# Kernel optimization log

Measured on AMD Instinct MI355X. Metric: run time of the kernel, lower is better.

The kernel has to match this reference:

```python
import jax, jax.numpy as jnp
import numpy as np

C = 512
G = 32  # groups
EPS = 1e-6

def setup_inputs() -> dict:
    key = jax.random.key(0)
    ks = jax.random.split(key, 12)
    x = jax.random.normal(ks[0], (2, C, 64, 64), dtype=jnp.float32)
    s = 1.0 / np.sqrt(C)
    params = {
        'gn_scale': jnp.ones((C,), jnp.float32),
        'gn_bias': jnp.zeros((C,), jnp.float32),
        'wq': jax.random.normal(ks[1], (C, C), jnp.float32) * s,
        'bq': jax.random.normal(ks[2], (C,), jnp.float32) * 0.01,
        'wk': jax.random.normal(ks[3], (C, C), jnp.float32) * s,
        'bk': jax.random.normal(ks[4], (C,), jnp.float32) * 0.01,
        'wv': jax.random.normal(ks[5], (C, C), jnp.float32) * s,
        'bv': jax.random.normal(ks[6], (C,), jnp.float32) * 0.01,
        'wp': jax.random.normal(ks[7], (C, C), jnp.float32) * s,
        'bp': jax.random.normal(ks[8], (C,), jnp.float32) * 0.01,
    }
    return {'x': x, **params}


def _group_norm(x, scale, bias):
    b, c, h, w = x.shape
    xg = x.reshape(b, G, c // G, h, w)
    mean = jnp.mean(xg, axis=(2, 3, 4), keepdims=True)
    var = jnp.var(xg, axis=(2, 3, 4), keepdims=True)
    xg = (xg - mean) * jax.lax.rsqrt(var + EPS)
    x = xg.reshape(b, c, h, w)
    return x * scale[None, :, None, None] + bias[None, :, None, None]


def _conv1x1(x, w, bias):
    # x: [b,c,h,w], w: [out,in] -> [b,out,h,w]
    return jnp.einsum('oc,bchw->bohw', w, x) + bias[None, :, None, None]


def reference(x, gn_scale, gn_bias, wq, bq, wk, bk, wv, bv, wp, bp):
    h = _group_norm(x, gn_scale, gn_bias)
    q = _conv1x1(h, wq, bq)
    k = _conv1x1(h, wk, bk)
    v = _conv1x1(h, wv, bv)
    b, c, h_, w_ = q.shape
    n = h_ * w_
    q = q.reshape(b, c, n)
    k = k.reshape(b, c, n)
    v = v.reshape(b, c, n)
    # attn[b,i,j] = sum_c q[b,c,i] k[b,c,j] * c^-0.5
    attn = jnp.einsum('bci,bcj->bij', q, k) * (c ** -0.5)
    attn = jax.nn.softmax(attn, axis=2)
    # out[b,c,i] = sum_j v[b,c,j] attn[b,i,j]
    out = jnp.einsum('bcj,bij->bci', v, attn)
    out = out.reshape(b, c, h_, w_)
    out = _conv1x1(out, wp, bp)
    return x + out
```

## Files before the change

### kernel.cpp

```cpp
#include <hip/hip_runtime.h>
#include <stdint.h>

typedef short short8 __attribute__((ext_vector_type(8)));
typedef short short4v __attribute__((ext_vector_type(4)));
typedef float f32x4 __attribute__((ext_vector_type(4)));
typedef float float4v __attribute__((ext_vector_type(4)));

__device__ inline float bf2f(short s) {
    union { unsigned u; float f; } c;
    c.u = ((unsigned)(unsigned short)s) << 16;
    return c.f;
}
__device__ inline short f2bf(float f) {
    union { float f; unsigned u; } c;
    c.f = f;
    unsigned u = c.u;
    unsigned r = (u + 0x7fffu + ((u >> 16) & 1u)) >> 16;
    return (short)r;
}

typedef const __attribute__((address_space(1))) char GChar;
typedef __attribute__((address_space(3))) char LChar;
__device__ __forceinline__ void gload_lds16(const void* g, void* l) {
    __builtin_amdgcn_global_load_lds((GChar*)g, (LChar*)l, 16, 0, 0);
}

template<int N> __device__ __forceinline__ void wait_vm() {
    if constexpr (N == 0)      asm volatile("s_waitcnt vmcnt(0)" ::: "memory");
    else if constexpr (N == 4) asm volatile("s_waitcnt vmcnt(4)" ::: "memory");
    else if constexpr (N == 6) asm volatile("s_waitcnt vmcnt(6)" ::: "memory");
    else static_assert(N == 0 || N == 4 || N == 6, "unsupported vmcnt");
}

__device__ __forceinline__ void wait_lgkm0() {
    asm volatile("s_waitcnt lgkmcnt(0)" ::: "memory");
}
__device__ __forceinline__ void wait_lgkm8() {
    asm volatile("s_waitcnt lgkmcnt(8)" ::: "memory");
}

__device__ __forceinline__ void phase_barrier() {
    __builtin_amdgcn_s_barrier();
    asm volatile("" ::: "memory");
}

__device__ __forceinline__ void swz_xy(int& bx, int& by) {
    int gx = gridDim.x;
    int nwg = gx * gridDim.y;
    int wg = by * gx + bx;
    int chunk = nwg >> 3;
    int swz = (wg & 7) * chunk + (wg >> 3);
    bx = swz % gx;
    by = swz / gx;
}

__global__ __launch_bounds__(256) void conv_w4(const float* __restrict__ w0, const float* __restrict__ w1,
                                               const float* __restrict__ w2, const float* __restrict__ w3,
                                               short* __restrict__ dst, float s0,
                                               float* __restrict__ rowsum,
                                               const float* __restrict__ bq, const float* __restrict__ bk,
                                               float* __restrict__ bqk, float* __restrict__ statsraw) {
    int gid = blockIdx.x * 256 + threadIdx.x;
    if (gid < 8192) rowsum[gid] = 0.0f;
    if (gid < 128)  statsraw[gid] = 0.0f;
    if (gid < 1024) bqk[gid] = (gid < 512) ? bq[gid] * s0 : bk[gid - 512];
    int idx = gid * 4;
    int wi = idx >> 18;
    int off = idx & 262143;
    const float* src = (wi == 0) ? w0 : (wi == 1) ? w1 : (wi == 2) ? w2 : w3;
    float sc = (wi == 0) ? s0 : 1.0f;
    float4v v = *reinterpret_cast<const float4v*>(src + off);
    short4v o;
    o[0] = f2bf(v[0] * sc); o[1] = f2bf(v[1] * sc);
    o[2] = f2bf(v[2] * sc); o[3] = f2bf(v[3] * sc);
    *reinterpret_cast<short4v*>(dst + idx) = o;
}

__global__ __launch_bounds__(256) void gn_stats2(const float* __restrict__ x, float* __restrict__ statsraw) {
    int bg = blockIdx.x;
    const float* p = x + (size_t)bg * 65536 + blockIdx.y * 8192;
    float s = 0.f, ss = 0.f;
    #pragma unroll
    for (int i = threadIdx.x * 4; i < 8192; i += 1024) {
        float4v q = *reinterpret_cast<const float4v*>(p + i);
        s  += q[0] + q[1] + q[2] + q[3];
        ss += q[0]*q[0] + q[1]*q[1] + q[2]*q[2] + q[3]*q[3];
    }
    #pragma unroll
    for (int off = 32; off >= 1; off >>= 1) {
        s  += __shfl_xor(s, off);
        ss += __shfl_xor(ss, off);
    }
    __shared__ float rs[8];
    int w = threadIdx.x >> 6, lane = threadIdx.x & 63;
    if (lane == 0) { rs[w] = s; rs[4 + w] = ss; }
    __syncthreads();
    if (threadIdx.x == 0) {
        float S1 = rs[0] + rs[1] + rs[2] + rs[3];
        float S2 = rs[4] + rs[5] + rs[6] + rs[7];
        atomicAdd(&statsraw[bg * 2],     S1);
        atomicAdd(&statsraw[bg * 2 + 1], S2);
    }
}

__global__ __launch_bounds__(256) void gn_apply_t(const float* __restrict__ x, const float* __restrict__ statsraw,
                                                  const float* __restrict__ scale, const float* __restrict__ bias,
                                                  short* __restrict__ hT) {
    __shared__ float t[64][65];
    int n0 = blockIdx.x * 64, c0 = blockIdx.y * 64, b = blockIdx.z;
    const float* xb = x + (size_t)b * 512 * 4096;
    int col = threadIdx.x & 63, rb = threadIdx.x >> 6;
    #pragma unroll
    for (int r = 0; r < 16; ++r) {
        int cl = rb + r * 4;
        int c = c0 + cl;
        int g = c >> 4;
        float sum   = statsraw[(b * 32 + g) * 2];
        float sumsq = statsraw[(b * 32 + g) * 2 + 1];
        float mean = sum * (1.f / 65536.f);
        float var  = sumsq * (1.f / 65536.f) - mean * mean;
        float rstd = rsqrtf(var + 1e-6f);
        float v = xb[(size_t)c * 4096 + n0 + col];
        t[col][cl] = (v - mean) * rstd * scale[c] + bias[c];
    }
    __syncthreads();
    short* hb = hT + (size_t)b * 4096 * 512;
    #pragma unroll
    for (int r = 0; r < 16; ++r) {
        int nl = rb + r * 4;
        hb[(size_t)(n0 + nl) * 512 + c0 + col] = f2bf(t[nl][col]);
    }
}

template<int EPI>
__global__ __launch_bounds__(512, 2) void gemm8b(
    const short* __restrict__ A, int zdiv, long sAb1, long sAb2, int lda,
    const short* __restrict__ B, long sBb1, long sBb2, int ldb,
    short* __restrict__ C, long sCb1, long sCb2, int ldc,
    int K, float* __restrict__ rowsum)
{
    __shared__ __align__(16) char lds[131072];

    const int tid = threadIdx.x;
    int bx = blockIdx.x, by = blockIdx.y;
    swz_xy(bx, by);
    const int bm = bx * 256, bn = by * 256;
    const int zb = blockIdx.z / zdiv, zs = blockIdx.z % zdiv;

    const short* Ab = A + (size_t)zb * sAb1 + (size_t)zs * sAb2;
    const short* Bb = B + (size_t)zb * sBb1 + (size_t)zs * sBb2;

    const int w = tid >> 6, lane = tid & 63;
    const int wm = w >> 2, wn = w & 3;
    const int l15 = lane & 15, l4 = lane >> 4;

    long srcAh[2][2], srcBh[2][2]; int dstAh[2][2], dstBh[2][2];
    #pragma unroll
    for (int h = 0; h < 2; ++h) {
        #pragma unroll
        for (int i = 0; i < 2; ++i) {
            int ch = i * 512 + tid;
            int r = h * 128 + (ch >> 3), c = ch & 7;
            srcAh[h][i] = (long)(bm + r) * lda + ((c ^ (r & 7)) << 3);
            dstAh[h][i] = r * 128 + c * 16;
            srcBh[h][i] = (long)(bn + r) * ldb + ((c ^ (r & 7)) << 3);
            dstBh[h][i] = 32768 + r * 128 + c * 16;
        }
    }
    auto stageAh = [&](int buf, int h, long kt) {
        char* l = lds + buf * 65536;
        gload_lds16(Ab + srcAh[h][0] + kt, l + dstAh[h][0]);
        gload_lds16(Ab + srcAh[h][1] + kt, l + dstAh[h][1]);
    };
    auto stageBh = [&](int buf, int h, long kt) {
        char* l = lds + buf * 65536;
        gload_lds16(Bb + srcBh[h][0] + kt, l + dstBh[h][0]);
        gload_lds16(Bb + srcBh[h][1] + kt, l + dstBh[h][1]);
    };

    auto fragA = [&](const char* base, int m, int ks) -> short8 {
        int r = wm * 128 + m * 16 + l15;
        int kk = ks * 4 + l4;
        return *reinterpret_cast<const short8*>(base + r * 128 + ((kk * 16) ^ ((r & 7) << 4)));
    };
    auto fragB = [&](const char* base, int n, int ks) -> short8 {
        int r = wn * 64 + n * 16 + l15;
        int kk = ks * 4 + l4;
        return *reinterpret_cast<const short8*>(base + 32768 + r * 128 + ((kk * 16) ^ ((r & 7) << 4)));
    };

    f32x4 acc[8][4] = {};
    const int nk = K >> 6;

    stageBh(0, 0, 0); stageBh(0, 1, 0);
    stageAh(0, 0, 0); stageAh(0, 1, 0);
    if (nk > 1) {
        stageBh(1, 0, 64); stageBh(1, 1, 64);
        wait_vm<4>();
    } else {
        wait_vm<0>();
    }
    phase_barrier();

    short8 bf[4][2];

    for (int t = 0; t < nk; ++t) {
        const char* lr = lds + (t & 1) * 65536;
        const int bufN = (t & 1) ^ 1;
        const int bufT = (t & 1);
        const long ktA = (long)(t + 1) << 6;
        const long ktB = (long)(t + 2) << 6;
        const bool pA = (t + 1 < nk);
        const bool pB = (t + 2 < nk);
        short8 a00, a01, a10, a11;

        #pragma unroll
        for (int n = 0; n < 4; ++n) { bf[n][0] = fragB(lr, n, 0); bf[n][1] = fragB(lr, n, 1); }
        a00 = fragA(lr, 0, 0); a01 = fragA(lr, 0, 1);
        a10 = fragA(lr, 1, 0); a11 = fragA(lr, 1, 1);
        if (pA) stageAh(bufN, 0, ktA);
        wait_lgkm8();
        phase_barrier();
        wait_lgkm0();
        __builtin_amdgcn_s_setprio(1);
        #pragma unroll
        for (int n = 0; n < 4; ++n) {
            acc[0][n] = __builtin_amdgcn_mfma_f32_16x16x32_bf16(a00, bf[n][0], acc[0][n], 0, 0, 0);
            acc[0][n] = __builtin_amdgcn_mfma_f32_16x16x32_bf16(a01, bf[n][1], acc[0][n], 0, 0, 0);
            acc[1][n] = __builtin_amdgcn_mfma_f32_16x16x32_bf16(a10, bf[n][0], acc[1][n], 0, 0, 0);
            acc[1][n] = __builtin_amdgcn_mfma_f32_16x16x32_bf16(a11, bf[n][1], acc[1][n], 0, 0, 0);
        }
        __builtin_amdgcn_s_setprio(0);
        __builtin_amdgcn_sched_barrier(0);
        phase_barrier();

        a00 = fragA(lr, 2, 0); a01 = fragA(lr, 2, 1);
        a10 = fragA(lr, 3, 0); a11 = fragA(lr, 3, 1);
        if (pA) stageAh(bufN, 1, ktA);
        phase_barrier();
        wait_lgkm0();
        __builtin_amdgcn_s_setprio(1);
        #pragma unroll
        for (int n = 0; n < 4; ++n) {
            acc[2][n] = __builtin_amdgcn_mfma_f32_16x16x32_bf16(a00, bf[n][0], acc[2][n], 0, 0, 0);
            acc[2][n] = __builtin_amdgcn_mfma_f32_16x16x32_bf16(a01, bf[n][1], acc[2][n], 0, 0, 0);
            acc[3][n] = __builtin_amdgcn_mfma_f32_16x16x32_bf16(a10, bf[n][0], acc[3][n], 0, 0, 0);
            acc[3][n] = __builtin_amdgcn_mfma_f32_16x16x32_bf16(a11, bf[n][1], acc[3][n], 0, 0, 0);
        }
        __builtin_amdgcn_s_setprio(0);
        __builtin_amdgcn_sched_barrier(0);
        phase_barrier();

        a00 = fragA(lr, 4, 0); a01 = fragA(lr, 4, 1);
        a10 = fragA(lr, 5, 0); a11 = fragA(lr, 5, 1);
        if (pB) stageBh(bufT, 0, ktB);
        phase_barrier();
        wait_lgkm0();
        __builtin_amdgcn_s_setprio(1);
        #pragma unroll
        for (int n = 0; n < 4; ++n) {
            acc[4][n] = __builtin_amdgcn_mfma_f32_16x16x32_bf16(a00, bf[n][0], acc[4][n], 0, 0, 0);
            acc[4][n] = __builtin_amdgcn_mfma_f32_16x16x32_bf16(a01, bf[n][1], acc[4][n], 0, 0, 0);
            acc[5][n] = __builtin_amdgcn_mfma_f32_16x16x32_bf16(a10, bf[n][0], acc[5][n], 0, 0, 0);
            acc[5][n] = __builtin_amdgcn_mfma_f32_16x16x32_bf16(a11, bf[n][1], acc[5][n], 0, 0, 0);
        }
        __builtin_amdgcn_s_setprio(0);
        __builtin_amdgcn_sched_barrier(0);
        phase_barrier();

        a00 = fragA(lr, 6, 0); a01 = fragA(lr, 6, 1);
        a10 = fragA(lr, 7, 0); a11 = fragA(lr, 7, 1);
        if (pB) stageBh(bufT, 1, ktB);
        if (pB)      wait_vm<4>();
        else if (pA) wait_vm<0>();
        phase_barrier();
        wait_lgkm0();
        __builtin_amdgcn_s_setprio(1);
        #pragma unroll
        for (int n = 0; n < 4; ++n) {
            acc[6][n] = __builtin_amdgcn_mfma_f32_16x16x32_bf16(a00, bf[n][0], acc[6][n], 0, 0, 0);
            acc[6][n] = __builtin_amdgcn_mfma_f32_16x16x32_bf16(a01, bf[n][1], acc[6][n], 0, 0, 0);
            acc[7][n] = __builtin_amdgcn_mfma_f32_16x16x32_bf16(a10, bf[n][0], acc[7][n], 0, 0, 0);
            acc[7][n] = __builtin_amdgcn_mfma_f32_16x16x32_bf16(a11, bf[n][1], acc[7][n], 0, 0, 0);
        }
        __builtin_amdgcn_s_setprio(0);
        __builtin_amdgcn_sched_barrier(0);
        phase_barrier();
    }

    short* Cb = C + (size_t)zb * sCb1 + (size_t)zs * sCb2;
    if constexpr (EPI == 0) {
        #pragma unroll
        for (int m = 0; m < 8; ++m) {
            #pragma unroll
            for (int r = 0; r < 4; ++r) {
                int row = bm + wm * 128 + m * 16 + l4 * 4 + r;
                #pragma unroll
                for (int n = 0; n < 4; ++n) {
                    int col = bn + wn * 64 + n * 16 + l15;
                    Cb[(size_t)row * ldc + col] = f2bf(acc[m][n][r]);
                }
            }
        }
    } else if constexpr (EPI == 2) {
        #pragma unroll
        for (int m = 0; m < 8; ++m) {
            #pragma unroll
            for (int r = 0; r < 4; ++r) {
                int row = bm + wm * 128 + m * 16 + l4 * 4 + r;
                float inv = 1.0f / rowsum[zb * 4096 + row];
                #pragma unroll
                for (int n = 0; n < 4; ++n) {
                    int col = bn + wn * 64 + n * 16 + l15;
                    Cb[(size_t)row * ldc + col] = f2bf(acc[m][n][r] * inv);
                }
            }
        }
    } else {
        float* lsum = (float*)lds;
        #pragma unroll
        for (int m = 0; m < 8; ++m) {
            #pragma unroll
            for (int r = 0; r < 4; ++r) {
                int lrow = wm * 128 + m * 16 + l4 * 4 + r;
                int row = bm + lrow;
                float part = 0.0f;
                #pragma unroll
                for (int n = 0; n < 4; ++n) {
                    int col = bn + wn * 64 + n * 16 + l15;
                    float e = __expf(acc[m][n][r]);
                    part += e;
                    Cb[(size_t)row * ldc + col] = f2bf(e);
                }
                part += __shfl_xor(part, 1);
                part += __shfl_xor(part, 2);
                part += __shfl_xor(part, 4);
                part += __shfl_xor(part, 8);
                if (l15 == 0) lsum[wn * 256 + lrow] = part;
            }
        }
        __syncthreads();
        if (tid < 256) {
            float s = (lsum[tid] + lsum[256 + tid]) + (lsum[512 + tid] + lsum[768 + tid]);
            atomicAdd(&rowsum[zb * 4096 + bm + tid], s);
        }
    }
}

template<int BMT, int BNT, int WM, int WN>
__global__ __launch_bounds__(512) void gemm_nt3(
    const short* __restrict__ A, int zdiv, long sAb1, long sAb2, int lda,
    const short* __restrict__ B, long sBb1, long sBb2, int ldb,
    void* __restrict__ Cv, long sCb1, long sCb2, int ldc,
    int K,
    const float* __restrict__ bias, int bias_mode,
    const float* __restrict__ res, long sResb,
    int c_fp32)
{
    constexpr int BUFB = (BMT + BNT) * 128;
    constexpr int ALPT = BMT / 64;
    constexpr int BLPT = BNT / 64;
    constexpr int MF   = BMT / WM / 16;
    constexpr int NF   = BNT / WN / 16;
    __shared__ __align__(16) char lds[2 * BUFB];

    const int tid = threadIdx.x;
    int bx = blockIdx.x, by = blockIdx.y;
    swz_xy(bx, by);
    const int bm = bx * BMT;
    const int bn = by * BNT;
    const int bz = blockIdx.z;
    const int zb = bz / zdiv, zs = bz % zdiv;

    const short* Ab = A + (size_t)zb * sAb1 + (size_t)zs * sAb2;
    const short* Bb = B + (size_t)zb * sBb1 + (size_t)zs * sBb2;

    const int w = tid >> 6;
    const int lane = tid & 63;
    const int wm = w / WN, wn = w % WN;
    const int wr = wm * (BMT / WM);
    const int wc = wn * (BNT / WN);

    f32x4 acc[MF][NF] = {};
    const int nk = K >> 6;

    auto stage = [&](int buf, int kt) {
        char* la = lds + buf * BUFB;
        char* lb = la + BMT * 128;
        #pragma unroll
        for (int i = 0; i < ALPT; ++i) {
            int ch = i * 512 + tid;
            int r = ch >> 3, c = ch & 7;
            gload_lds16(Ab + (size_t)(bm + r) * lda + kt + ((c ^ (r & 7)) << 3), la + ch * 16);
        }
        #pragma unroll
        for (int i = 0; i < BLPT; ++i) {
            int ch = i * 512 + tid;
            int r = ch >> 3, c = ch & 7;
            gload_lds16(Bb + (size_t)(bn + r) * ldb + kt + ((c ^ (r & 7)) << 3), lb + ch * 16);
        }
    };

    stage(0, 0);
    int cur = 0;
    for (int t = 0; t < nk; ++t) {
        if (t + 1 < nk) {
            stage(cur ^ 1, (t + 1) << 6);
            wait_vm<6>();
        } else {
            wait_vm<0>();
        }
        phase_barrier();

        const char* la = lds + cur * BUFB;
        const char* lb = la + BMT * 128;
        #pragma unroll
        for (int ks = 0; ks < 2; ++ks) {
            const int kb = ks * 64 + (lane >> 4) * 16;
            short8 af[MF], bfv[NF];
            #pragma unroll
            for (int m = 0; m < MF; ++m) {
                int r = wr + m * 16 + (lane & 15);
                af[m] = *reinterpret_cast<const short8*>(la + r * 128 + (kb ^ ((r & 7) << 4)));
            }
            #pragma unroll
            for (int n = 0; n < NF; ++n) {
                int r = wc + n * 16 + (lane & 15);
                bfv[n] = *reinterpret_cast<const short8*>(lb + r * 128 + (kb ^ ((r & 7) << 4)));
            }
            #pragma unroll
            for (int m = 0; m < MF; ++m)
                #pragma unroll
                for (int n = 0; n < NF; ++n)
                    acc[m][n] = __builtin_amdgcn_mfma_f32_16x16x32_bf16(af[m], bfv[n], acc[m][n], 0, 0, 0);
        }
        asm volatile("" ::: "memory");
        __builtin_amdgcn_s_barrier();
        cur ^= 1;
    }

    const int row0 = (lane >> 4) * 4;
    const int col0 = lane & 15;
    short* Cb16 = (short*)Cv + (size_t)zb * sCb1 + (size_t)zs * sCb2;
    float* Cf32 = (float*)Cv + (size_t)zb * sCb1 + (size_t)zs * sCb2;
    const float* resb = res ? res + (size_t)zb * sResb : nullptr;

    #pragma unroll
    for (int m = 0; m < MF; ++m) {
        #pragma unroll
        for (int r = 0; r < 4; ++r) {
            int row = bm + wr + m * 16 + row0 + r;
            float bvr = (bias_mode == 1) ? bias[row] : 0.0f;
            #pragma unroll
            for (int n = 0; n < NF; ++n) {
                int col = bn + wc + n * 16 + col0;
                float v = acc[m][n][r];
                if (bias_mode == 1) v += bvr;
                else if (bias_mode == 2) v += bias[col];
                size_t idx = (size_t)row * ldc + col;
                if (c_fp32) {
                    if (resb) v += resb[idx];
                    Cf32[idx] = v;
                } else {
                    Cb16[idx] = f2bf(v);
                }
            }
        }
    }
}

template<int BNT>
__global__ __launch_bounds__(256) void gemm_nt2(
    const short* __restrict__ A, long sAb, int lda,
    const short* __restrict__ B, long sBb, int ldb,
    void* __restrict__ Cv, long sCb, int ldc,
    int K,
    const float* __restrict__ bias, int bias_mode,
    const float* __restrict__ res, long sResb,
    int c_fp32)
{
    constexpr int BMT = 128;
    constexpr int NF  = BNT / 32;
    constexpr int BUF = (BMT + BNT) * 128;
    constexpr int ALPT = (BMT * 8) / 256;
    constexpr int BLPT = (BNT * 8) / 256;
    __shared__ __align__(16) char lds[2 * BUF];

    const int tid = threadIdx.x;
    int bx = blockIdx.x, by = blockIdx.y;
    swz_xy(bx, by);
    const int bm = bx * BMT;
    const int bn = by * BNT;
    const int bz = blockIdx.z;

    const short* Ab = A + (size_t)bz * sAb;
    const short* Bb = B + (size_t)bz * sBb;

    const int w = tid >> 6;
    const int lane = tid & 63;
    const int wr = (w >> 1) * 64;
    const int wc = (w & 1) * (BNT / 2);

    f32x4 acc[4][NF] = {};
    const int nk = K >> 6;

    auto stage = [&](int buf, int kt) {
        char* la = lds + buf * BUF;
        char* lb = la + BMT * 128;
        #pragma unroll
        for (int i = 0; i < ALPT; ++i) {
            int ch = i * 256 + tid;
            int r = ch >> 3, c = ch & 7;
            gload_lds16(Ab + (size_t)(bm + r) * lda + kt + ((c ^ (r & 7)) << 3), la + ch * 16);
        }
        #pragma unroll
        for (int i = 0; i < BLPT; ++i) {
            int ch = i * 256 + tid;
            int r = ch >> 3, c = ch & 7;
            gload_lds16(Bb + (size_t)(bn + r) * ldb + kt + ((c ^ (r & 7)) << 3), lb + ch * 16);
        }
    };

    stage(0, 0);
    int cur = 0;
    for (int t = 0; t < nk; ++t) {
        if (t + 1 < nk) {
            stage(cur ^ 1, (t + 1) << 6);
            wait_vm<6>();
        } else {
            wait_vm<0>();
        }
        phase_barrier();

        const char* la = lds + cur * BUF;
        const char* lb = la + BMT * 128;
        #pragma unroll
        for (int ks = 0; ks < 2; ++ks) {
            const int kb = ks * 64 + (lane >> 4) * 16;
            short8 af[4], bfv[NF];
            #pragma unroll
            for (int m = 0; m < 4; ++m) {
                int r = wr + m * 16 + (lane & 15);
                af[m] = *reinterpret_cast<const short8*>(la + r * 128 + (kb ^ ((r & 7) << 4)));
            }
            #pragma unroll
            for (int n = 0; n < NF; ++n) {
                int r = wc + n * 16 + (lane & 15);
                bfv[n] = *reinterpret_cast<const short8*>(lb + r * 128 + (kb ^ ((r & 7) << 4)));
            }
            #pragma unroll
            for (int m = 0; m < 4; ++m)
                #pragma unroll
                for (int n = 0; n < NF; ++n)
                    acc[m][n] = __builtin_amdgcn_mfma_f32_16x16x32_bf16(af[m], bfv[n], acc[m][n], 0, 0, 0);
        }
        asm volatile("" ::: "memory");
        __builtin_amdgcn_s_barrier();
        cur ^= 1;
    }

    const int row0 = (lane >> 4) * 4;
    const int col0 = lane & 15;
    short* Cb16 = (short*)Cv + (size_t)bz * sCb;
    float* Cf32 = (float*)Cv + (size_t)bz * sCb;
    const float* resb = res ? res + (size_t)bz * sResb : nullptr;

    #pragma unroll
    for (int m = 0; m < 4; ++m) {
        #pragma unroll
        for (int r = 0; r < 4; ++r) {
            int row = bm + wr + m * 16 + row0 + r;
            float bvr = (bias_mode == 1) ? bias[row] : 0.0f;
            #pragma unroll
            for (int n = 0; n < NF; ++n) {
                int col = bn + wc + n * 16 + col0;
                float v = acc[m][n][r];
                if (bias_mode == 1) v += bvr;
                else if (bias_mode == 2) v += bias[col];
                size_t idx = (size_t)row * ldc + col;
                if (c_fp32) {
                    if (resb) v += resb[idx];
                    Cf32[idx] = v;
                } else {
                    Cb16[idx] = f2bf(v);
                }
            }
        }
    }
}

__global__ __launch_bounds__(256) void gemm_out(
    const short* __restrict__ A,
    const short* __restrict__ part, long sPz, long sPb,
    float* __restrict__ Cout, long sCb, int ldc,
    const float* __restrict__ bias,
    const float* __restrict__ res, long sResb)
{
    constexpr int BMT = 128, BNT = 64;
    constexpr int BUF = (BMT + BNT) * 128;
    __shared__ __align__(16) char lds[2 * BUF];

    const int tid = threadIdx.x;
    int bx = blockIdx.x, by = blockIdx.y;
    swz_xy(bx, by);
    const int bm = bx * BMT;
    const int bn = by * BNT;
    const int bz = blockIdx.z;

    const short* Pb = part + (size_t)bz * sPb;

    const int w = tid >> 6;
    const int lane = tid & 63;
    const int wr = (w >> 1) * 64;
    const int wc = (w & 1) * 32;

    f32x4 acc[4][2] = {};
    const int nk = 8;

    long srcA[4]; int dstA[4];
    #pragma unroll
    for (int i = 0; i < 4; ++i) {
        int ch = i * 256 + tid;
        int r = ch >> 3, c = ch & 7;
        srcA[i] = (long)(bm + r) * 512 + ((c ^ (r & 7)) << 3);
        dstA[i] = ch * 16;
    }
    long srcB[2]; int dstB[2];
    #pragma unroll
    for (int i = 0; i < 2; ++i) {
        int ch = i * 256 + tid;
        int r = ch >> 3, c = ch & 7;
        srcB[i] = (long)(bn + r) * 512 + c * 8;
        dstB[i] = BMT * 128 + r * 128 + ((c * 16) ^ ((r & 7) << 4));
    }

    auto stageA = [&](int buf, long kt) {
        char* la = lds + buf * BUF;
        #pragma unroll
        for (int i = 0; i < 4; ++i) gload_lds16(A + srcA[i] + kt, la + dstA[i]);
    };
    auto loadB = [&](long kt, short8 rv[2][4]) {
        #pragma unroll
        for (int i = 0; i < 2; ++i)
            #pragma unroll
            for (int z = 0; z < 4; ++z)
                rv[i][z] = *reinterpret_cast<const short8*>(Pb + z * sPz + srcB[i] + kt);
    };
    auto writeB = [&](int buf, short8 rv[2][4]) {
        char* l = lds + buf * BUF;
        #pragma unroll
        for (int i = 0; i < 2; ++i) {
            short8 o;
            #pragma unroll
            for (int j = 0; j < 8; ++j)
                o[j] = f2bf((bf2f(rv[i][0][j]) + bf2f(rv[i][1][j])) +
                            (bf2f(rv[i][2][j]) + bf2f(rv[i][3][j])));
            *reinterpret_cast<short8*>(l + dstB[i]) = o;
        }
    };

    short8 rv[2][4];
    stageA(0, 0);
    loadB(0, rv);
    writeB(0, rv);
    __syncthreads();

    int cur = 0;
    for (int t = 0; t < nk; ++t) {
        const bool pA = (t + 1 < nk);
        if (pA) {
            stageA(cur ^ 1, (long)(t + 1) << 6);
            loadB((long)(t + 1) << 6, rv);
        }
        const char* la = lds + cur * BUF;
        const char* lb = la + BMT * 128;
        #pragma unroll
        for (int ks = 0; ks < 2; ++ks) {
            const int kb = ks * 64 + (lane >> 4) * 16;
            short8 af[4], bfv[2];
            #pragma unroll
            for (int m = 0; m < 4; ++m) {
                int r = wr + m * 16 + (lane & 15);
                af[m] = *reinterpret_cast<const short8*>(la + r * 128 + (kb ^ ((r & 7) << 4)));
            }
            #pragma unroll
            for (int n = 0; n < 2; ++n) {
                int r = wc + n * 16 + (lane & 15);
                bfv[n] = *reinterpret_cast<const short8*>(lb + r * 128 + (kb ^ ((r & 7) << 4)));
            }
            #pragma unroll
            for (int m = 0; m < 4; ++m)
                #pragma unroll
                for (int n = 0; n < 2; ++n)
                    acc[m][n] = __builtin_amdgcn_mfma_f32_16x16x32_bf16(af[m], bfv[n], acc[m][n], 0, 0, 0);
        }
        if (pA) writeB(cur ^ 1, rv);
        __syncthreads();
        cur ^= 1;
    }

    const int row0 = (lane >> 4) * 4;
    const int col0 = lane & 15;
    float* Cb = Cout + (size_t)bz * sCb;
    const float* resb = res + (size_t)bz * sResb;

    #pragma unroll
    for (int m = 0; m < 4; ++m) {
        #pragma unroll
        for (int r = 0; r < 4; ++r) {
            int row = bm + wr + m * 16 + row0 + r;
            float bvr = bias[row];
            #pragma unroll
            for (int n = 0; n < 2; ++n) {
                int col = bn + wc + n * 16 + col0;
                size_t idx = (size_t)row * ldc + col;
                Cb[idx] = acc[m][n][r] + bvr + resb[idx];
            }
        }
    }
}

extern "C" void kernel_launch(void* const* d_in, const int* in_sizes, int n_in,
                              void* d_out, int out_size, void* d_ws, size_t ws_size,
                              hipStream_t stream) {
    (void)in_sizes; (void)n_in; (void)out_size; (void)ws_size;
    const float* x        = (const float*)d_in[0];
    const float* gn_scale = (const float*)d_in[1];
    const float* gn_bias  = (const float*)d_in[2];
    const float* wq = (const float*)d_in[3];
    const float* bq = (const float*)d_in[4];
    const float* wk = (const float*)d_in[5];
    const float* bk = (const float*)d_in[6];
    const float* wv = (const float*)d_in[7];
    const float* bv = (const float*)d_in[8];
    const float* wp = (const float*)d_in[9];
    const float* bp = (const float*)d_in[10];

    char* ws = (char*)d_ws;
    const size_t MB = 1024 * 1024;
    short* hT   = (short*)(ws + 0);
    short* QKT  = (short*)(ws + 8   * MB);
    short* V    = (short*)(ws + 24  * MB);
    short* S    = (short*)(ws + 40  * MB);
    short* part = (short*)(ws + 104 * MB);
    short* wB   = (short*)(ws + 168 * MB);
    float* statsraw = (float*)(ws + 170 * MB);
    float* bqk  = (float*)(ws + 170 * MB + 4096);
    float* rowsum = (float*)(ws + 171 * MB);

    const long NC   = 4096L * 512L;
    const long CN   = 512L * 4096L;
    const long QKNC = 4096L * 1024L;
    const long SNN  = 4096L * 4096L;
    const float attn_scale = 0.044194173824159216f;

    conv_w4<<<1024, 256, 0, stream>>>(wq, wk, wv, wp, wB, attn_scale, rowsum,
                                      bq, bk, bqk, statsraw);

    gn_stats2<<<dim3(64, 8), 256, 0, stream>>>(x, statsraw);
    gn_apply_t<<<dim3(64, 8, 2), 256, 0, stream>>>(x, statsraw, gn_scale, gn_bias, hT);

    gemm_nt3<128, 256, 2, 4><<<dim3(32, 4, 2), 512, 0, stream>>>(
        hT, 1, NC, 0, 512, wB, 0, 0, 512, QKT, QKNC, 0, 1024, 512, bqk, 2, nullptr, 0, 0);
    gemm_nt2<64><<<dim3(4, 64, 2), 256, 0, stream>>>(
        wB + 524288, 0, 512, hT, NC, 512, V, CN, 4096, 512, bv, 1, nullptr, 0, 0);

    gemm8b<1><<<dim3(16, 16, 2), 512, 0, stream>>>(
        QKT, 1, QKNC, 0, 1024, QKT + 512, QKNC, 0, 1024, S, SNN, 0, 4096, 512, rowsum);
    gemm8b<2><<<dim3(16, 2, 8), 512, 0, stream>>>(
        S, 4, SNN, 1024, 4096, V, CN, 1024, 4096, part, 4L * NC, NC, 512, 1024, rowsum);

    gemm_out<<<dim3(4, 64, 2), 256, 0, stream>>>(
        wB + 786432, part, NC, 4L * NC, (float*)d_out, CN, 4096, bp, x, CN);
}
```

Before: 156.2 us.

## Fuse Q, K and V projections into one gemm8b launch with transposed V epilogue

Replaces the separate QK projection GEMM and the V projection GEMM with a single 256x256-tile gemm8b launch over a concatenated 1536-wide weight. The bias for all three projections is packed into one buffer, and a new epilogue writes Q and K row-major while scattering V transposed into its channel-major buffer. The intent is to drop one launch and read the normalized activations once instead of twice. The cost is that the transposed V stores are strided rather than coalesced, and the 192-block grid may underfill the device.

```diff
diff --git a/kernel.cpp b/kernel.cpp
--- a/kernel.cpp
+++ b/kernel.cpp
@@ -59,11 +59,13 @@
                                                short* __restrict__ dst, float s0,
                                                float* __restrict__ rowsum,
                                                const float* __restrict__ bq, const float* __restrict__ bk,
-                                               float* __restrict__ bqk, float* __restrict__ statsraw) {
+                                               const float* __restrict__ bv,
+                                               float* __restrict__ bqkv, float* __restrict__ statsraw) {
     int gid = blockIdx.x * 256 + threadIdx.x;
     if (gid < 8192) rowsum[gid] = 0.0f;
     if (gid < 128)  statsraw[gid] = 0.0f;
-    if (gid < 1024) bqk[gid] = (gid < 512) ? bq[gid] * s0 : bk[gid - 512];
+    if (gid < 1536) bqkv[gid] = (gid < 512) ? bq[gid] * s0
+                               : (gid < 1024) ? bk[gid - 512] : bv[gid - 1024];
     int idx = gid * 4;
     int wi = idx >> 18;
     int off = idx & 262143;
@@ -137,7 +139,8 @@
     const short* __restrict__ A, int zdiv, long sAb1, long sAb2, int lda,
     const short* __restrict__ B, long sBb1, long sBb2, int ldb,
     short* __restrict__ C, long sCb1, long sCb2, int ldc,
-    int K, float* __restrict__ rowsum)
+    int K, float* __restrict__ rowsum,
+    const float* __restrict__ cbias, short* __restrict__ vout)
 {
     __shared__ __align__(16) char lds[131072];
 
@@ -313,6 +316,25 @@
                 for (int n = 0; n < 4; ++n) {
                     int col = bn + wn * 64 + n * 16 + l15;
                     Cb[(size_t)row * ldc + col] = f2bf(acc[m][n][r] * inv);
+                }
+            }
+        }
+    } else if constexpr (EPI == 3) {
+        short* Vb = vout + (size_t)zb * (512L * 4096L);
+        #pragma unroll
+        for (int m = 0; m < 8; ++m) {
+            #pragma unroll
+            for (int r = 0; r < 4; ++r) {
+                int row = bm + wm * 128 + m * 16 + l4 * 4 + r;
+                #pragma unroll
+                for (int n = 0; n < 4; ++n) {
+                    int col = bn + wn * 64 + n * 16 + l15;
+                    float v = acc[m][n][r] + cbias[col];
+                    if (bn < 1024) {
+                        Cb[(size_t)row * ldc + col] = f2bf(v);
+                    } else {
+                        Vb[(size_t)(col - 1024) * 4096 + row] = f2bf(v);
+                    }
                 }
             }
         }
@@ -347,248 +369,6 @@
     }
 }
 
-template<int BMT, int BNT, int WM, int WN>
-__global__ __launch_bounds__(512) void gemm_nt3(
-    const short* __restrict__ A, int zdiv, long sAb1, long sAb2, int lda,
-    const short* __restrict__ B, long sBb1, long sBb2, int ldb,
-    void* __restrict__ Cv, long sCb1, long sCb2, int ldc,
-    int K,
-    const float* __restrict__ bias, int bias_mode,
-    const float* __restrict__ res, long sResb,
-    int c_fp32)
-{
-    constexpr int BUFB = (BMT + BNT) * 128;
-    constexpr int ALPT = BMT / 64;
-    constexpr int BLPT = BNT / 64;
-    constexpr int MF   = BMT / WM / 16;
-    constexpr int NF   = BNT / WN / 16;
-    __shared__ __align__(16) char lds[2 * BUFB];
-
-    const int tid = threadIdx.x;
-    int bx = blockIdx.x, by = blockIdx.y;
-    swz_xy(bx, by);
-    const int bm = bx * BMT;
-    const int bn = by * BNT;
-    const int bz = blockIdx.z;
-    const int zb = bz / zdiv, zs = bz % zdiv;
-
-    const short* Ab = A + (size_t)zb * sAb1 + (size_t)zs * sAb2;
-    const short* Bb = B + (size_t)zb * sBb1 + (size_t)zs * sBb2;
-
-    const int w = tid >> 6;
-    const int lane = tid & 63;
-    const int wm = w / WN, wn = w % WN;
-    const int wr = wm * (BMT / WM);
-    const int wc = wn * (BNT / WN);
-
-    f32x4 acc[MF][NF] = {};
-    const int nk = K >> 6;
-
-    auto stage = [&](int buf, int kt) {
-        char* la = lds + buf * BUFB;
-        char* lb = la + BMT * 128;
-        #pragma unroll
-        for (int i = 0; i < ALPT; ++i) {
-            int ch = i * 512 + tid;
-            int r = ch >> 3, c = ch & 7;
-            gload_lds16(Ab + (size_t)(bm + r) * lda + kt + ((c ^ (r & 7)) << 3), la + ch * 16);
-        }
-        #pragma unroll
-        for (int i = 0; i < BLPT; ++i) {
-            int ch = i * 512 + tid;
-            int r = ch >> 3, c = ch & 7;
-            gload_lds16(Bb + (size_t)(bn + r) * ldb + kt + ((c ^ (r & 7)) << 3), lb + ch * 16);
-        }
-    };
-
-    stage(0, 0);
-    int cur = 0;
-    for (int t = 0; t < nk; ++t) {
-        if (t + 1 < nk) {
-            stage(cur ^ 1, (t + 1) << 6);
-            wait_vm<6>();
-        } else {
-            wait_vm<0>();
-        }
-        phase_barrier();
-
-        const char* la = lds + cur * BUFB;
-        const char* lb = la + BMT * 128;
-        #pragma unroll
-        for (int ks = 0; ks < 2; ++ks) {
-            const int kb = ks * 64 + (lane >> 4) * 16;
-            short8 af[MF], bfv[NF];
-            #pragma unroll
-            for (int m = 0; m < MF; ++m) {
-                int r = wr + m * 16 + (lane & 15);
-                af[m] = *reinterpret_cast<const short8*>(la + r * 128 + (kb ^ ((r & 7) << 4)));
-            }
-            #pragma unroll
-            for (int n = 0; n < NF; ++n) {
-                int r = wc + n * 16 + (lane & 15);
-                bfv[n] = *reinterpret_cast<const short8*>(lb + r * 128 + (kb ^ ((r & 7) << 4)));
-            }
-            #pragma unroll
-            for (int m = 0; m < MF; ++m)
-                #pragma unroll
-                for (int n = 0; n < NF; ++n)
-                    acc[m][n] = __builtin_amdgcn_mfma_f32_16x16x32_bf16(af[m], bfv[n], acc[m][n], 0, 0, 0);
-        }
-        asm volatile("" ::: "memory");
-        __builtin_amdgcn_s_barrier();
-        cur ^= 1;
-    }
-
-    const int row0 = (lane >> 4) * 4;
-    const int col0 = lane & 15;
-    short* Cb16 = (short*)Cv + (size_t)zb * sCb1 + (size_t)zs * sCb2;
-    float* Cf32 = (float*)Cv + (size_t)zb * sCb1 + (size_t)zs * sCb2;
-    const float* resb = res ? res + (size_t)zb * sResb : nullptr;
-
-    #pragma unroll
-    for (int m = 0; m < MF; ++m) {
-        #pragma unroll
-        for (int r = 0; r < 4; ++r) {
-            int row = bm + wr + m * 16 + row0 + r;
-            float bvr = (bias_mode == 1) ? bias[row] : 0.0f;
-            #pragma unroll
-            for (int n = 0; n < NF; ++n) {
-                int col = bn + wc + n * 16 + col0;
-                float v = acc[m][n][r];
-                if (bias_mode == 1) v += bvr;
-                else if (bias_mode == 2) v += bias[col];
-                size_t idx = (size_t)row * ldc + col;
-                if (c_fp32) {
-                    if (resb) v += resb[idx];
-                    Cf32[idx] = v;
-                } else {
-                    Cb16[idx] = f2bf(v);
-                }
-            }
-        }
-    }
-}
-
-template<int BNT>
-__global__ __launch_bounds__(256) void gemm_nt2(
-    const short* __restrict__ A, long sAb, int lda,
-    const short* __restrict__ B, long sBb, int ldb,
-    void* __restrict__ Cv, long sCb, int ldc,
-    int K,
-    const float* __restrict__ bias, int bias_mode,
-    const float* __restrict__ res, long sResb,
-    int c_fp32)
-{
-    constexpr int BMT = 128;
-    constexpr int NF  = BNT / 32;
-    constexpr int BUF = (BMT + BNT) * 128;
-    constexpr int ALPT = (BMT * 8) / 256;
-    constexpr int BLPT = (BNT * 8) / 256;
-    __shared__ __align__(16) char lds[2 * BUF];
-
-    const int tid = threadIdx.x;
-    int bx = blockIdx.x, by = blockIdx.y;
-    swz_xy(bx, by);
-    const int bm = bx * BMT;
-    const int bn = by * BNT;
-    const int bz = blockIdx.z;
-
-    const short* Ab = A + (size_t)bz * sAb;
-    const short* Bb = B + (size_t)bz * sBb;
-
-    const int w = tid >> 6;
-    const int lane = tid & 63;
-    const int wr = (w >> 1) * 64;
-    const int wc = (w & 1) * (BNT / 2);
-
-    f32x4 acc[4][NF] = {};
-    const int nk = K >> 6;
-
-    auto stage = [&](int buf, int kt) {
-        char* la = lds + buf * BUF;
-        char* lb = la + BMT * 128;
-        #pragma unroll
-        for (int i = 0; i < ALPT; ++i) {
-            int ch = i * 256 + tid;
-            int r = ch >> 3, c = ch & 7;
-            gload_lds16(Ab + (size_t)(bm + r) * lda + kt + ((c ^ (r & 7)) << 3), la + ch * 16);
-        }
-        #pragma unroll
-        for (int i = 0; i < BLPT; ++i) {
-            int ch = i * 256 + tid;
-            int r = ch >> 3, c = ch & 7;
-            gload_lds16(Bb + (size_t)(bn + r) * ldb + kt + ((c ^ (r & 7)) << 3), lb + ch * 16);
-        }
-    };
-
-    stage(0, 0);
-    int cur = 0;
-    for (int t = 0; t < nk; ++t) {
-        if (t + 1 < nk) {
-            stage(cur ^ 1, (t + 1) << 6);
-            wait_vm<6>();
-        } else {
-            wait_vm<0>();
-        }
-        phase_barrier();
-
-        const char* la = lds + cur * BUF;
-        const char* lb = la + BMT * 128;
-        #pragma unroll
-        for (int ks = 0; ks < 2; ++ks) {
-            const int kb = ks * 64 + (lane >> 4) * 16;
-            short8 af[4], bfv[NF];
-            #pragma unroll
-            for (int m = 0; m < 4; ++m) {
-                int r = wr + m * 16 + (lane & 15);
-                af[m] = *reinterpret_cast<const short8*>(la + r * 128 + (kb ^ ((r & 7) << 4)));
-            }
-            #pragma unroll
-            for (int n = 0; n < NF; ++n) {
-                int r = wc + n * 16 + (lane & 15);
-                bfv[n] = *reinterpret_cast<const short8*>(lb + r * 128 + (kb ^ ((r & 7) << 4)));
-            }
-            #pragma unroll
-            for (int m = 0; m < 4; ++m)
-                #pragma unroll
-                for (int n = 0; n < NF; ++n)
-                    acc[m][n] = __builtin_amdgcn_mfma_f32_16x16x32_bf16(af[m], bfv[n], acc[m][n], 0, 0, 0);
-        }
-        asm volatile("" ::: "memory");
-        __builtin_amdgcn_s_barrier();
-        cur ^= 1;
-    }
-
-    const int row0 = (lane >> 4) * 4;
-    const int col0 = lane & 15;
-    short* Cb16 = (short*)Cv + (size_t)bz * sCb;
-    float* Cf32 = (float*)Cv + (size_t)bz * sCb;
-    const float* resb = res ? res + (size_t)bz * sResb : nullptr;
-
-    #pragma unroll
-    for (int m = 0; m < 4; ++m) {
-        #pragma unroll
-        for (int r = 0; r < 4; ++r) {
-            int row = bm + wr + m * 16 + row0 + r;
-            float bvr = (bias_mode == 1) ? bias[row] : 0.0f;
-            #pragma unroll
-            for (int n = 0; n < NF; ++n) {
-                int col = bn + wc + n * 16 + col0;
-                float v = acc[m][n][r];
-                if (bias_mode == 1) v += bvr;
-                else if (bias_mode == 2) v += bias[col];
-                size_t idx = (size_t)row * ldc + col;
-                if (c_fp32) {
-                    if (resb) v += resb[idx];
-                    Cf32[idx] = v;
-                } else {
-                    Cb16[idx] = f2bf(v);
-                }
-            }
-        }
-    }
-}
-
 __global__ __launch_bounds__(256) void gemm_out(
     const short* __restrict__ A,
     const short* __restrict__ part, long sPz, long sPb,
@@ -739,36 +519,37 @@
     char* ws = (char*)d_ws;
     const size_t MB = 1024 * 1024;
     short* hT   = (short*)(ws + 0);
-    short* QKT  = (short*)(ws + 8   * MB);
-    short* V    = (short*)(ws + 24  * MB);
+    short* QKV  = (short*)(ws + 8   * MB);
+    short* V    = (short*)(ws + 32  * MB);
     short* S    = (short*)(ws + 40  * MB);
     short* part = (short*)(ws + 104 * MB);
     short* wB   = (short*)(ws + 168 * MB);
     float* statsraw = (float*)(ws + 170 * MB);
-    float* bqk  = (float*)(ws + 170 * MB + 4096);
+    float* bqkv = (float*)(ws + 170 * MB + 4096);
     float* rowsum = (float*)(ws + 171 * MB);
 
-    const long NC   = 4096L * 512L;
-    const long CN   = 512L * 4096L;
-    const long QKNC = 4096L * 1024L;
-    const long SNN  = 4096L * 4096L;
+    const long NC    = 4096L * 512L;
+    const long CN    = 512L * 4096L;
+    const long QKVN  = 4096L * 1536L;
+    const long SNN   = 4096L * 4096L;
     const float attn_scale = 0.044194173824159216f;
 
     conv_w4<<<1024, 256, 0, stream>>>(wq, wk, wv, wp, wB, attn_scale, rowsum,
-                                      bq, bk, bqk, statsraw);
+                                      bq, bk, bv, bqkv, statsraw);
 
     gn_stats2<<<dim3(64, 8), 256, 0, stream>>>(x, statsraw);
     gn_apply_t<<<dim3(64, 8, 2), 256, 0, stream>>>(x, statsraw, gn_scale, gn_bias, hT);
 
-    gemm_nt3<128, 256, 2, 4><<<dim3(32, 4, 2), 512, 0, stream>>>(
-        hT, 1, NC, 0, 512, wB, 0, 0, 512, QKT, QKNC, 0, 1024, 512, bqk, 2, nullptr, 0, 0);
-    gemm_nt2<64><<<dim3(4, 64, 2), 256, 0, stream>>>(
-        wB + 524288, 0, 512, hT, NC, 512, V, CN, 4096, 512, bv, 1, nullptr, 0, 0);
+    gemm8b<3><<<dim3(16, 6, 2), 512, 0, stream>>>(
+        hT, 1, NC, 0, 512, wB, 0, 0, 512, QKV, QKVN, 0, 1536, 512,
+        nullptr, bqkv, V);
 
     gemm8b<1><<<dim3(16, 16, 2), 512, 0, stream>>>(
-        QKT, 1, QKNC, 0, 1024, QKT + 512, QKNC, 0, 1024, S, SNN, 0, 4096, 512, rowsum);
+        QKV, 1, QKVN, 0, 1536, QKV + 512, QKVN, 0, 1536, S, SNN, 0, 4096, 512,
+        rowsum, nullptr, nullptr);
     gemm8b<2><<<dim3(16, 2, 8), 512, 0, stream>>>(
-        S, 4, SNN, 1024, 4096, V, CN, 1024, 4096, part, 4L * NC, NC, 512, 1024, rowsum);
+        S, 4, SNN, 1024, 4096, V, CN, 1024, 4096, part, 4L * NC, NC, 512, 1024,
+        rowsum, nullptr, nullptr);
 
     gemm_out<<<dim3(4, 64, 2), 256, 0, stream>>>(
         wB + 786432, part, NC, 4L * NC, (float*)d_out, CN, 4096, bp, x, CN);
```

Result: slower. 166.1 us (+6.3%).
